# Kernel optimization log

Hardware: AMD Instinct MI355X
Metric: run time of the kernel (lower is better)

The kernel has to match this reference:

```python
import jax, jax.numpy as jnp
import numpy as np

N_NODES = 50000
N_EDGES = 400000
HIDDEN = 128
OUT_DIM = 1
N_LAYERS = 3
NUM_GRAPHS = 64
VOCAB = 101


def _lin(x, w, b):
    return x @ w + b


def setup_inputs() -> dict:
    key = jax.random.key(0)
    ks = jax.random.split(key, 20)
    inp = {}
    inp['z'] = jax.random.randint(ks[0], (N_NODES,), 0, VOCAB)
    inp['edge_index'] = jax.random.randint(ks[1], (2, N_EDGES), 0, N_NODES)
    inp['edge_attr'] = jax.random.normal(ks[2], (N_EDGES, 1), dtype=jnp.float32)
    inp['batch'] = jnp.sort(jax.random.randint(ks[3], (N_NODES,), 0, NUM_GRAPHS))
    s = 0.05
    inp['embed'] = jax.random.normal(ks[4], (VOCAB, HIDDEN), dtype=jnp.float32) * s
    # per-layer stacked params; weights stored [in, out]
    inp['msg_w1'] = jax.random.normal(ks[5], (N_LAYERS, 2 * HIDDEN + 1, HIDDEN), dtype=jnp.float32) * s
    inp['msg_b1'] = jnp.zeros((N_LAYERS, HIDDEN), dtype=jnp.float32)
    inp['msg_w2'] = jax.random.normal(ks[6], (N_LAYERS, HIDDEN, HIDDEN), dtype=jnp.float32) * s
    inp['msg_b2'] = jnp.zeros((N_LAYERS, HIDDEN), dtype=jnp.float32)
    inp['upd_w1'] = jax.random.normal(ks[7], (N_LAYERS, 2 * HIDDEN, HIDDEN), dtype=jnp.float32) * s
    inp['upd_b1'] = jnp.zeros((N_LAYERS, HIDDEN), dtype=jnp.float32)
    inp['upd_w2'] = jax.random.normal(ks[8], (N_LAYERS, HIDDEN, HIDDEN), dtype=jnp.float32) * s
    inp['upd_b2'] = jnp.zeros((N_LAYERS, HIDDEN), dtype=jnp.float32)
    inp['head_w1'] = jax.random.normal(ks[9], (HIDDEN, HIDDEN), dtype=jnp.float32) * s
    inp['head_b1'] = jnp.zeros((HIDDEN,), dtype=jnp.float32)
    inp['head_w2'] = jax.random.normal(ks[10], (HIDDEN, OUT_DIM), dtype=jnp.float32) * s
    inp['head_b2'] = jnp.zeros((OUT_DIM,), dtype=jnp.float32)
    return inp


def reference(z, edge_index, edge_attr, batch, embed, msg_w1, msg_b1, msg_w2, msg_b2,
              upd_w1, upd_b1, upd_w2, upd_b2, head_w1, head_b1, head_w2, head_b2):
    src, dst = edge_index[0], edge_index[1]
    h = embed[z]  # [N, H]
    for l in range(N_LAYERS):
        m_in = jnp.concatenate([h[src], h[dst], edge_attr], axis=1)  # [E, 2H+1]
        msg = _lin(jax.nn.relu(_lin(m_in, msg_w1[l], msg_b1[l])), msg_w2[l], msg_b2[l])
        agg = jax.ops.segment_sum(msg, dst, num_segments=N_NODES)  # [N, H]
        upd_in = jnp.concatenate([h, agg], axis=1)  # [N, 2H]
        h = h + _lin(jax.nn.relu(_lin(upd_in, upd_w1[l], upd_b1[l])), upd_w2[l], upd_b2[l])
    pooled = jax.ops.segment_sum(h, batch, num_segments=NUM_GRAPHS)
    counts = jax.ops.segment_sum(jnp.ones((h.shape[0], 1), h.dtype), batch, num_segments=NUM_GRAPHS)
    pooled = pooled / jnp.maximum(counts, 1.0)
    return _lin(jax.nn.relu(_lin(pooled, head_w1, head_b1)), head_w2, head_b2)
```

## Files before the change

kernel.cpp:

```cpp
#include <hip/hip_runtime.h>

#define N_NODES 50000
#define NPAD 50048
#define N_EDGES 400000
#define HID 128
#define NUM_GRAPHS 64
#define SCAN_B 196
#define ECAP 2048

typedef __bf16 bf16;
typedef bf16 bf16x8 __attribute__((ext_vector_type(8)));
typedef float f32x4 __attribute__((ext_vector_type(4)));

__device__ inline bf16x8 cvt8(const float* p) {
    const float4 a = *(const float4*)p;
    const float4 b = *(const float4*)(p + 4);
    bf16x8 v;
    v[0] = (bf16)a.x; v[1] = (bf16)a.y; v[2] = (bf16)a.z; v[3] = (bf16)a.w;
    v[4] = (bf16)b.x; v[5] = (bf16)b.y; v[6] = (bf16)b.z; v[7] = (bf16)b.w;
    return v;
}

__device__ __forceinline__ void tile_out(const bf16* lds, bf16* g, int n0, int tid) {
    #pragma unroll
    for (int u = 0; u < 4; ++u) {
        const int unit = u * 256 + tid;
        const int row = unit >> 4;
        const int ci = (unit & 15) * 8;
        *(bf16x8*)&g[(size_t)(n0 + row) * HID + ci] =
            *(const bf16x8*)&lds[row * 136 + ci];
    }
}

__global__ void k_hist(const int* __restrict__ edst, int* __restrict__ deg) {
    int e = blockIdx.x * 256 + threadIdx.x;
    if (e < N_EDGES) atomicAdd(&deg[edst[e]], 1);
}

__global__ void k_scan1(const int* __restrict__ deg, int* __restrict__ partial) {
    __shared__ int buf[256];
    int i = blockIdx.x * 256 + threadIdx.x;
    buf[threadIdx.x] = (i < N_NODES) ? deg[i] : 0;
    __syncthreads();
    for (int off = 128; off > 0; off >>= 1) {
        if (threadIdx.x < off) buf[threadIdx.x] += buf[threadIdx.x + off];
        __syncthreads();
    }
    if (threadIdx.x == 0) partial[blockIdx.x] = buf[0];
}

__global__ void k_scan2(int* __restrict__ partial, int* __restrict__ row_ptr) {
    __shared__ int buf[256];
    int v = (threadIdx.x < SCAN_B) ? partial[threadIdx.x] : 0;
    buf[threadIdx.x] = v;
    __syncthreads();
    for (int off = 1; off < 256; off <<= 1) {
        int t = (threadIdx.x >= off) ? buf[threadIdx.x - off] : 0;
        __syncthreads();
        buf[threadIdx.x] += t;
        __syncthreads();
    }
    if (threadIdx.x < SCAN_B) partial[threadIdx.x] = buf[threadIdx.x] - v;
    if (threadIdx.x == 255) row_ptr[N_NODES] = buf[255];
}

__global__ void k_scan3(const int* __restrict__ deg, const int* __restrict__ partial,
                        int* __restrict__ row_ptr, int* __restrict__ cursor) {
    __shared__ int buf[256];
    int i = blockIdx.x * 256 + threadIdx.x;
    int v = (i < N_NODES) ? deg[i] : 0;
    buf[threadIdx.x] = v;
    __syncthreads();
    for (int off = 1; off < 256; off <<= 1) {
        int t = (threadIdx.x >= off) ? buf[threadIdx.x - off] : 0;
        __syncthreads();
        buf[threadIdx.x] += t;
        __syncthreads();
    }
    if (i < N_NODES) {
        int ex = partial[blockIdx.x] + buf[threadIdx.x] - v;
        row_ptr[i] = ex;
        cursor[i] = ex;
    }
}

__global__ void k_scatter(const int* __restrict__ esrc, const int* __restrict__ edst,
                          const float* __restrict__ attr, int* __restrict__ cursor,
                          int* __restrict__ s_src, float* __restrict__ s_attr) {
    int e = blockIdx.x * 256 + threadIdx.x;
    if (e >= N_EDGES) return;
    int p = atomicAdd(&cursor[edst[e]], 1);
    s_src[p] = esrc[e];
    s_attr[p] = attr[e];
}

__global__ void k_wprep(const float* __restrict__ msg_w1, const float* __restrict__ upd_w1,
                        const float* __restrict__ upd_w2,
                        bf16* __restrict__ W1t, bf16* __restrict__ U1t,
                        bf16* __restrict__ U2t) {
    const int l = blockIdx.y;
    const int n = blockIdx.x, k = threadIdx.x;
    const float* w1  = msg_w1 + (size_t)l * 257 * HID;
    const float* uw1 = upd_w1 + (size_t)l * 2 * HID * HID;
    const float* uw2 = upd_w2 + (size_t)l * HID * HID;
    if (n < 256) {
        W1t[(size_t)l * 256 * HID + n * HID + k] =
            (bf16)w1[(size_t)((n & 128) + k) * HID + (n & 127)];
    } else if (n < 384) {
        const int nn = n - 256;
        U1t[(size_t)l * HID * HID + nn * HID + k] = (bf16)uw1[(size_t)k * HID + nn];
    } else {
        const int nn = n - 384;
        U2t[(size_t)l * HID * HID + nn * HID + k] = (bf16)uw2[(size_t)k * HID + nn];
    }
}

__global__ void k_small(const float* __restrict__ msg_w2, const float* __restrict__ upd_w1,
                        const float* __restrict__ msg_b2,
                        bf16* __restrict__ W2Ut, float* __restrict__ b2u) {
    __shared__ float row[HID];
    const int l = blockIdx.y;
    const int k = blockIdx.x, j = threadIdx.x;
    const float* w2  = msg_w2 + (size_t)l * HID * HID;
    const float* uw1 = upd_w1 + (size_t)l * 2 * HID * HID;
    const float* b2  = msg_b2 + (size_t)l * HID;
    const float* src = (k < HID) ? &w2[(size_t)k * HID] : b2;
    row[j] = src[j];
    __syncthreads();
    float acc = 0.f;
    #pragma unroll 8
    for (int m = 0; m < HID; ++m)
        acc = fmaf(row[m], uw1[(size_t)(HID + m) * HID + j], acc);
    if (k < HID) W2Ut[(size_t)l * HID * HID + (size_t)j * HID + k] = (bf16)acc;
    else b2u[l * HID + j] = acc;
}

__launch_bounds__(256, 4)
__global__ void k_embed_pre(const int* __restrict__ z, const float* __restrict__ embed,
                            const bf16* __restrict__ W1t, const float* __restrict__ b1,
                            bf16* __restrict__ h16, bf16* __restrict__ P, bf16* __restrict__ Q) {
    __shared__ bf16 sH[64 * 136];
    __shared__ bf16 sH2[64 * 136];
    const int tid = threadIdx.x;
    const int n0 = blockIdx.x * 64;
    {
        const int r = tid & 63, cg = tid >> 6;
        const int n = n0 + r;
        const bool valid = n < N_NODES;
        const float* src = valid ? &embed[(size_t)z[n] * HID + cg * 32] : embed;
        #pragma unroll
        for (int i = 0; i < 4; ++i) {
            bf16x8 v;
            if (valid) {
                v = cvt8(src + i * 8);
            } else {
                for (int j = 0; j < 8; ++j) v[j] = (bf16)0.f;
            }
            *(bf16x8*)&sH[r * 136 + cg * 32 + i * 8] = v;
        }
    }
    __syncthreads();
    tile_out(sH, h16, n0, tid);

    const int lane = tid & 63, wave = tid >> 6;
    const int lr = lane & 15, kq = (lane >> 4) * 8, rq = (lane >> 4) * 4;
    const int bcol = wave * 64;

    const f32x4 z4 = {0.f, 0.f, 0.f, 0.f};
    f32x4 acc[4][4];
    #pragma unroll
    for (int mi = 0; mi < 4; ++mi)
        #pragma unroll
        for (int ni = 0; ni < 4; ++ni) acc[mi][ni] = z4;

    #pragma unroll
    for (int ks = 0; ks < 4; ++ks) {
        bf16x8 av[4], bv[4];
        #pragma unroll
        for (int mi = 0; mi < 4; ++mi)
            av[mi] = *(const bf16x8*)&sH[(mi * 16 + lr) * 136 + ks * 32 + kq];
        #pragma unroll
        for (int ni = 0; ni < 4; ++ni)
            bv[ni] = *(const bf16x8*)&W1t[(size_t)(bcol + ni * 16 + lr) * HID + ks * 32 + kq];
        #pragma unroll
        for (int mi = 0; mi < 4; ++mi)
            #pragma unroll
            for (int ni = 0; ni < 4; ++ni)
                acc[mi][ni] = __builtin_amdgcn_mfma_f32_16x16x32_bf16(av[mi], bv[ni],
                                                                      acc[mi][ni], 0, 0, 0);
    }
    __syncthreads();

    {
        bf16* sOut = (bcol < 128) ? sH : sH2;
        const int cb = bcol & 127;
        #pragma unroll
        for (int ni = 0; ni < 4; ++ni) {
            const int c = cb + ni * 16 + lr;
            const float bias = (bcol >= 128) ? b1[c] : 0.f;
            #pragma unroll
            for (int mi = 0; mi < 4; ++mi)
                #pragma unroll
                for (int r = 0; r < 4; ++r)
                    sOut[(mi * 16 + rq + r) * 136 + c] = (bf16)(acc[mi][ni][r] + bias);
        }
    }
    __syncthreads();
    tile_out(sH, P, n0, tid);
    tile_out(sH2, Q, n0, tid);
}

template<int DO_PRE>
__launch_bounds__(256, 4)
__global__ void k_layer(bf16* __restrict__ h16,
                        const bf16* __restrict__ P, const bf16* __restrict__ Q,
                        const int* __restrict__ row_ptr, const int* __restrict__ s_src,
                        const float* __restrict__ s_attr, const float* __restrict__ w1last,
                        const bf16* __restrict__ U1t, const bf16* __restrict__ W2Ut,
                        const float* __restrict__ ub1, const float* __restrict__ b2u,
                        const bf16* __restrict__ U2t, const float* __restrict__ ub2,
                        const bf16* __restrict__ W1tn, const float* __restrict__ b1n,
                        bf16* __restrict__ Pn, bf16* __restrict__ Qn) {
    __shared__ bf16 sAgg[64 * 136];
    __shared__ bf16 sT[64 * 136];
    __shared__ float sDeg[64];
    const int tid = threadIdx.x;
    const int n0 = blockIdx.x * 64;

    {
        int*   sEsrc = (int*)sT;
        float* sEatt = (float*)(sT + ECAP * 2);
        const int elo = row_ptr[n0];
        const int ehi = row_ptr[min(n0 + 64, N_NODES)];
        const int ecap = min(ehi - elo, ECAP);
        for (int i = tid; i < ecap; i += 256) {
            sEsrc[i] = s_src[elo + i];
            sEatt[i] = s_attr[elo + i];
        }
        __syncthreads();

        const int grp = tid >> 4, ln = tid & 15, c8 = ln * 8;
        float wl[8];
        #pragma unroll
        for (int j = 0; j < 8; ++j) wl[j] = w1last[c8 + j];
        #pragma unroll
        for (int t = 0; t < 4; ++t) {
            const int row = t * 16 + grp;
            const int n = n0 + row;
            float a8[8];
            #pragma unroll
            for (int j = 0; j < 8; ++j) a8[j] = 0.f;
            if (n < N_NODES) {
                const int lo = row_ptr[n], hi = row_ptr[n + 1];
                if (ln == 0) sDeg[row] = (float)(hi - lo);
                const bf16x8 qv = *(const bf16x8*)&Q[(size_t)n * HID + c8];
                float q8[8];
                #pragma unroll
                for (int j = 0; j < 8; ++j) q8[j] = (float)qv[j];
                const int llo = lo - elo, lhi = hi - elo;
                if (lhi <= ecap) {
                    int e = llo;
                    for (; e + 4 <= lhi; e += 4) {
                        const int s0 = sEsrc[e], s1 = sEsrc[e + 1];
                        const int s2 = sEsrc[e + 2], s3 = sEsrc[e + 3];
                        const float t0 = sEatt[e], t1 = sEatt[e + 1];
                        const float t2 = sEatt[e + 2], t3 = sEatt[e + 3];
                        const bf16x8 p0 = *(const bf16x8*)&P[(size_t)s0 * HID + c8];
                        const bf16x8 p1 = *(const bf16x8*)&P[(size_t)s1 * HID + c8];
                        const bf16x8 p2 = *(const bf16x8*)&P[(size_t)s2 * HID + c8];
                        const bf16x8 p3 = *(const bf16x8*)&P[(size_t)s3 * HID + c8];
                        #pragma unroll
                        for (int j = 0; j < 8; ++j) {
                            a8[j] += fmaxf(fmaf(t0, wl[j], q8[j] + (float)p0[j]), 0.f);
                            a8[j] += fmaxf(fmaf(t1, wl[j], q8[j] + (float)p1[j]), 0.f);
                            a8[j] += fmaxf(fmaf(t2, wl[j], q8[j] + (float)p2[j]), 0.f);
                            a8[j] += fmaxf(fmaf(t3, wl[j], q8[j] + (float)p3[j]), 0.f);
                        }
                    }
                    for (; e < lhi; ++e) {
                        const int s0 = sEsrc[e];
                        const float t0 = sEatt[e];
                        const bf16x8 p0 = *(const bf16x8*)&P[(size_t)s0 * HID + c8];
                        #pragma unroll
                        for (int j = 0; j < 8; ++j)
                            a8[j] += fmaxf(fmaf(t0, wl[j], q8[j] + (float)p0[j]), 0.f);
                    }
                } else {
                    for (int e = lo; e < hi; ++e) {
                        const int s0 = s_src[e];
                        const float t0 = s_attr[e];
                        const bf16x8 p0 = *(const bf16x8*)&P[(size_t)s0 * HID + c8];
                        #pragma unroll
                        for (int j = 0; j < 8; ++j)
                            a8[j] += fmaxf(fmaf(t0, wl[j], q8[j] + (float)p0[j]), 0.f);
                    }
                }
            } else if (ln == 0) {
                sDeg[row] = 0.f;
            }
            bf16x8 o;
            #pragma unroll
            for (int j = 0; j < 8; ++j) o[j] = (bf16)a8[j];
            *(bf16x8*)&sAgg[row * 136 + c8] = o;
        }
    }
    __syncthreads();

    const int lane = tid & 63, wave = tid >> 6;
    const int lr = lane & 15, kq = (lane >> 4) * 8, rq = (lane >> 4) * 4;
    const int nw = wave * 32;
    const f32x4 z4 = {0.f, 0.f, 0.f, 0.f};

    f32x4 acc[4][2];
    #pragma unroll
    for (int mi = 0; mi < 4; ++mi) { acc[mi][0] = z4; acc[mi][1] = z4; }

    #pragma unroll
    for (int ks = 0; ks < 4; ++ks) {
        bf16x8 av[4], bv[2];
        #pragma unroll
        for (int mi = 0; mi < 4; ++mi)
            av[mi] = *(const bf16x8*)&h16[(size_t)(n0 + mi * 16 + lr) * HID + ks * 32 + kq];
        #pragma unroll
        for (int ni = 0; ni < 2; ++ni)
            bv[ni] = *(const bf16x8*)&U1t[(size_t)(nw + ni * 16 + lr) * HID + ks * 32 + kq];
        #pragma unroll
        for (int mi = 0; mi < 4; ++mi)
            #pragma unroll
            for (int ni = 0; ni < 2; ++ni)
                acc[mi][ni] = __builtin_amdgcn_mfma_f32_16x16x32_bf16(av[mi], bv[ni],
                                                                      acc[mi][ni], 0, 0, 0);
    }
    #pragma unroll
    for (int ks = 0; ks < 4; ++ks) {
        bf16x8 av[4], bv[2];
        #pragma unroll
        for (int mi = 0; mi < 4; ++mi)
            av[mi] = *(const bf16x8*)&sAgg[(mi * 16 + lr) * 136 + ks * 32 + kq];
        #pragma unroll
        for (int ni = 0; ni < 2; ++ni)
            bv[ni] = *(const bf16x8*)&W2Ut[(size_t)(nw + ni * 16 + lr) * HID + ks * 32 + kq];
        #pragma unroll
        for (int mi = 0; mi < 4; ++mi)
            #pragma unroll
            for (int ni = 0; ni < 2; ++ni)
                acc[mi][ni] = __builtin_amdgcn_mfma_f32_16x16x32_bf16(av[mi], bv[ni],
                                                                      acc[mi][ni], 0, 0, 0);
    }
    __syncthreads();

    #pragma unroll
    for (int ni = 0; ni < 2; ++ni) {
        const int c = nw + ni * 16 + lr;
        const float bb1 = ub1[c], bb2 = b2u[c];
        #pragma unroll
        for (int mi = 0; mi < 4; ++mi)
            #pragma unroll
            for (int r = 0; r < 4; ++r) {
                const int row = mi * 16 + rq + r;
                float v = acc[mi][ni][r] + bb1 + sDeg[row] * bb2;
                sT[row * 136 + c] = (bf16)fmaxf(v, 0.f);
            }
    }
    __syncthreads();

    f32x4 acc2[4][2];
    #pragma unroll
    for (int mi = 0; mi < 4; ++mi) { acc2[mi][0] = z4; acc2[mi][1] = z4; }
    #pragma unroll
    for (int ks = 0; ks < 4; ++ks) {
        bf16x8 av[4], bv[2];
        #pragma unroll
        for (int mi = 0; mi < 4; ++mi)
            av[mi] = *(const bf16x8*)&sT[(mi * 16 + lr) * 136 + ks * 32 + kq];
        #pragma unroll
        for (int ni = 0; ni < 2; ++ni)
            bv[ni] = *(const bf16x8*)&U2t[(size_t)(nw + ni * 16 + lr) * HID + ks * 32 + kq];
        #pragma unroll
        for (int mi = 0; mi < 4; ++mi)
            #pragma unroll
            for (int ni = 0; ni < 2; ++ni)
                acc2[mi][ni] = __builtin_amdgcn_mfma_f32_16x16x32_bf16(av[mi], bv[ni],
                                                                       acc2[mi][ni], 0, 0, 0);
    }
    __syncthreads();

    #pragma unroll
    for (int ni = 0; ni < 2; ++ni) {
        const int c = nw + ni * 16 + lr;
        const float bb = ub2[c];
        #pragma unroll
        for (int mi = 0; mi < 4; ++mi)
            #pragma unroll
            for (int r = 0; r < 4; ++r) {
                const int row = mi * 16 + rq + r;
                const size_t off = (size_t)(n0 + row) * HID + c;
                const float nh = (float)h16[off] + acc2[mi][ni][r] + bb;
                sT[row * 136 + c] = (bf16)nh;
                if (DO_PRE) sAgg[row * 136 + c] = (bf16)nh;
            }
    }
    __syncthreads();
    tile_out(sT, h16, n0, tid);

    if (DO_PRE) {
        const int bcol = wave * 64;
        f32x4 pacc[4][4];
        #pragma unroll
        for (int mi = 0; mi < 4; ++mi)
            #pragma unroll
            for (int ni = 0; ni < 4; ++ni) pacc[mi][ni] = z4;

        #pragma unroll
        for (int ks = 0; ks < 4; ++ks) {
            bf16x8 av[4], bv[4];
            #pragma unroll
            for (int mi = 0; mi < 4; ++mi)
                av[mi] = *(const bf16x8*)&sAgg[(mi * 16 + lr) * 136 + ks * 32 + kq];
            #pragma unroll
            for (int ni = 0; ni < 4; ++ni)
                bv[ni] = *(const bf16x8*)&W1tn[(size_t)(bcol + ni * 16 + lr) * HID + ks * 32 + kq];
            #pragma unroll
            for (int mi = 0; mi < 4; ++mi)
                #pragma unroll
                for (int ni = 0; ni < 4; ++ni)
                    pacc[mi][ni] = __builtin_amdgcn_mfma_f32_16x16x32_bf16(av[mi], bv[ni],
                                                                           pacc[mi][ni], 0, 0, 0);
        }
        __syncthreads();

        {
            bf16* sOut = (bcol < 128) ? sT : sAgg;
            const int cb = bcol & 127;
            #pragma unroll
            for (int ni = 0; ni < 4; ++ni) {
                const int c = cb + ni * 16 + lr;
                const float bias = (bcol >= 128) ? b1n[c] : 0.f;
                #pragma unroll
                for (int mi = 0; mi < 4; ++mi)
                    #pragma unroll
                    for (int r = 0; r < 4; ++r)
                        sOut[(mi * 16 + rq + r) * 136 + c] = (bf16)(pacc[mi][ni][r] + bias);
            }
        }
        __syncthreads();
        tile_out(sT, Pn, n0, tid);
        tile_out(sAgg, Qn, n0, tid);
    }
}

__global__ void k_pool(const bf16* __restrict__ h16, const int* __restrict__ batch,
                       float* __restrict__ pooled) {
    const int n0 = blockIdx.x * 64;
    const int c = threadIdx.x & 127;
    const int half = threadIdx.x >> 7;
    int cur = -1;
    float s = 0.f;
    const int rbeg = n0 + half * 32;
    const int rend = min(rbeg + 32, N_NODES);
    for (int n = rbeg; n < rend; ++n) {
        const int g = batch[n];
        const float v = (float)h16[(size_t)n * HID + c];
        if (g != cur) {
            if (cur >= 0) atomicAdd(&pooled[cur * HID + c], s);
            cur = g; s = v;
        } else {
            s += v;
        }
    }
    if (cur >= 0) atomicAdd(&pooled[cur * HID + c], s);
}

__device__ inline int lb(const int* a, int n, int v) {
    int lo = 0, hi = n;
    while (lo < hi) { int m = (lo + hi) >> 1; if (a[m] < v) lo = m + 1; else hi = m; }
    return lo;
}

__global__ void k_head(const float* __restrict__ pooled, const int* __restrict__ batch,
                       const float* __restrict__ hw1, const float* __restrict__ hb1,
                       const float* __restrict__ hw2, const float* __restrict__ hb2,
                       float* __restrict__ out) {
    const int g = blockIdx.x;
    const int c = threadIdx.x;
    __shared__ float sp[HID];
    __shared__ float red[HID];
    __shared__ int sb[2];
    if (c == 0) { sb[0] = lb(batch, N_NODES, g); sb[1] = lb(batch, N_NODES, g + 1); }
    __syncthreads();
    const float cnt = fmaxf((float)(sb[1] - sb[0]), 1.f);
    sp[c] = pooled[g * HID + c] / cnt;
    __syncthreads();
    float acc = hb1[c];
    #pragma unroll 8
    for (int k = 0; k < HID; ++k) acc = fmaf(sp[k], hw1[k * HID + c], acc);
    red[c] = fmaxf(acc, 0.f) * hw2[c];
    __syncthreads();
    for (int s = 64; s > 0; s >>= 1) {
        if (c < s) red[c] += red[c + s];
        __syncthreads();
    }
    if (c == 0) out[g] = red[0] + hb2[0];
}

extern "C" void kernel_launch(void* const* d_in, const int* in_sizes, int n_in,
                              void* d_out, int out_size, void* d_ws, size_t ws_size,
                              hipStream_t stream) {
    const int*   z       = (const int*)d_in[0];
    const int*   ei      = (const int*)d_in[1];
    const float* eattr   = (const float*)d_in[2];
    const int*   batch   = (const int*)d_in[3];
    const float* embed   = (const float*)d_in[4];
    const float* msg_w1  = (const float*)d_in[5];
    const float* msg_b1  = (const float*)d_in[6];
    const float* msg_w2  = (const float*)d_in[7];
    const float* msg_b2  = (const float*)d_in[8];
    const float* upd_w1  = (const float*)d_in[9];
    const float* upd_b1  = (const float*)d_in[10];
    const float* upd_w2  = (const float*)d_in[11];
    const float* upd_b2  = (const float*)d_in[12];
    const float* head_w1 = (const float*)d_in[13];
    const float* head_b1 = (const float*)d_in[14];
    const float* head_w2 = (const float*)d_in[15];
    const float* head_b2 = (const float*)d_in[16];
    float* out = (float*)d_out;

    float* pooled = (float*)d_ws;
    float* b2u    = pooled + NUM_GRAPHS * HID;
    float* s_attr = b2u + 3 * HID;
    int* deg_i    = (int*)(s_attr + N_EDGES);
    int* row_ptr  = deg_i + N_NODES;
    int* partial  = row_ptr + N_NODES + 1;
    int* cursor   = partial + 256;
    int* s_src    = cursor + N_NODES;
    bf16* h16     = (bf16*)((((unsigned long long)(s_src + N_EDGES)) + 15ULL) & ~15ULL);
    bf16* P0      = h16 + (size_t)NPAD * HID;
    bf16* Q0      = P0 + (size_t)NPAD * HID;
    bf16* P1      = Q0 + (size_t)NPAD * HID;
    bf16* Q1      = P1 + (size_t)NPAD * HID;
    bf16* W1t     = Q1 + (size_t)NPAD * HID;
    bf16* U1t     = W1t + 3 * 256 * HID;
    bf16* W2Ut    = U1t + 3 * HID * HID;
    bf16* U2t     = W2Ut + 3 * HID * HID;

    const int* esrc = ei;
    const int* edst = ei + N_EDGES;

    hipMemsetAsync(deg_i, 0, N_NODES * sizeof(int), stream);
    k_hist<<<(N_EDGES + 255) / 256, 256, 0, stream>>>(edst, deg_i);
    k_scan1<<<SCAN_B, 256, 0, stream>>>(deg_i, partial);
    k_scan2<<<1, 256, 0, stream>>>(partial, row_ptr);
    k_scan3<<<SCAN_B, 256, 0, stream>>>(deg_i, partial, row_ptr, cursor);
    k_scatter<<<(N_EDGES + 255) / 256, 256, 0, stream>>>(esrc, edst, eattr, cursor, s_src, s_attr);
    {
        dim3 g1(512, 3);
        k_wprep<<<g1, 128, 0, stream>>>(msg_w1, upd_w1, upd_w2, W1t, U1t, U2t);
        dim3 g2(HID + 1, 3);
        k_small<<<g2, HID, 0, stream>>>(msg_w2, upd_w1, msg_b2, W2Ut, b2u);
    }

    const int nblk = NPAD / 64;
    k_embed_pre<<<nblk, 256, 0, stream>>>(z, embed, W1t, msg_b1, h16, P0, Q0);

    bf16* Pa = P0; bf16* Qa = Q0; bf16* Pb = P1; bf16* Qb = Q1;
    for (int l = 0; l < 3; ++l) {
        const float* w1last = msg_w1 + (size_t)l * 257 * HID + 256 * HID;
        const bf16* U1l  = U1t  + (size_t)l * HID * HID;
        const bf16* W2Ul = W2Ut + (size_t)l * HID * HID;
        const bf16* U2l  = U2t  + (size_t)l * HID * HID;
        if (l < 2) {
            k_layer<1><<<nblk, 256, 0, stream>>>(
                h16, Pa, Qa, row_ptr, s_src, s_attr, w1last,
                U1l, W2Ul, upd_b1 + (size_t)l * HID, b2u + l * HID,
                U2l, upd_b2 + (size_t)l * HID,
                W1t + (size_t)(l + 1) * 256 * HID, msg_b1 + (size_t)(l + 1) * HID, Pb, Qb);
            bf16* tp = Pa; Pa = Pb; Pb = tp;
            bf16* tq = Qa; Qa = Qb; Qb = tq;
        } else {
            k_layer<0><<<nblk, 256, 0, stream>>>(
                h16, Pa, Qa, row_ptr, s_src, s_attr, w1last,
                U1l, W2Ul, upd_b1 + (size_t)l * HID, b2u + l * HID,
                U2l, upd_b2 + (size_t)l * HID,
                nullptr, nullptr, nullptr, nullptr);
        }
    }
    hipMemsetAsync(pooled, 0, NUM_GRAPHS * HID * sizeof(float), stream);
    k_pool<<<nblk, 256, 0, stream>>>(h16, batch, pooled);
    k_head<<<NUM_GRAPHS, 128, 0, stream>>>(pooled, batch, head_w1, head_b1, head_w2, head_b2, out);
}
```

Baseline: 266.2 us.

## Fuse mean-pool into final layer kernel and unroll edge gather by eight

The final layer kernel now does the graph pooling directly from its shared-memory tile. This drops the separate pool kernel and the last write and re-read of h16. The edge aggregation loop also gains an 8-wide unrolled path so more independent P-row gathers are in flight, at the cost of extra register pressure. Row bounds are now guarded when reading h16 for padded rows.

```diff
diff --git a/kernel.cpp b/kernel.cpp
--- a/kernel.cpp
+++ b/kernel.cpp
@@ -220,7 +220,8 @@
                         const float* __restrict__ ub1, const float* __restrict__ b2u,
                         const bf16* __restrict__ U2t, const float* __restrict__ ub2,
                         const bf16* __restrict__ W1tn, const float* __restrict__ b1n,
-                        bf16* __restrict__ Pn, bf16* __restrict__ Qn) {
+                        bf16* __restrict__ Pn, bf16* __restrict__ Qn,
+                        const int* __restrict__ batch, float* __restrict__ pooled) {
     __shared__ bf16 sAgg[64 * 136];
     __shared__ bf16 sT[64 * 136];
     __shared__ float sDeg[64];
@@ -260,6 +261,21 @@
                 const int llo = lo - elo, lhi = hi - elo;
                 if (lhi <= ecap) {
                     int e = llo;
+                    for (; e + 8 <= lhi; e += 8) {
+                        int   ss[8];
+                        float tt[8];
+                        bf16x8 pp[8];
+                        #pragma unroll
+                        for (int u = 0; u < 8; ++u) { ss[u] = sEsrc[e + u]; tt[u] = sEatt[e + u]; }
+                        #pragma unroll
+                        for (int u = 0; u < 8; ++u)
+                            pp[u] = *(const bf16x8*)&P[(size_t)ss[u] * HID + c8];
+                        #pragma unroll
+                        for (int u = 0; u < 8; ++u)
+                            #pragma unroll
+                            for (int j = 0; j < 8; ++j)
+                                a8[j] += fmaxf(fmaf(tt[u], wl[j], q8[j] + (float)pp[u][j]), 0.f);
+                    }
                     for (; e + 4 <= lhi; e += 4) {
                         const int s0 = sEsrc[e], s1 = sEsrc[e + 1];
                         const int s2 = sEsrc[e + 2], s3 = sEsrc[e + 3];
@@ -394,16 +410,21 @@
             #pragma unroll
             for (int r = 0; r < 4; ++r) {
                 const int row = mi * 16 + rq + r;
-                const size_t off = (size_t)(n0 + row) * HID + c;
-                const float nh = (float)h16[off] + acc2[mi][ni][r] + bb;
+                const int gr = n0 + row;
+                float nh = 0.f;
+                if (gr < N_NODES) {
+                    const size_t off = (size_t)gr * HID + c;
+                    nh = (float)h16[off] + acc2[mi][ni][r] + bb;
+                }
                 sT[row * 136 + c] = (bf16)nh;
                 if (DO_PRE) sAgg[row * 136 + c] = (bf16)nh;
             }
     }
     __syncthreads();
-    tile_out(sT, h16, n0, tid);
 
     if (DO_PRE) {
+        tile_out(sT, h16, n0, tid);
+
         const int bcol = wave * 64;
         f32x4 pacc[4][4];
         #pragma unroll
@@ -446,29 +467,26 @@
         __syncthreads();
         tile_out(sT, Pn, n0, tid);
         tile_out(sAgg, Qn, n0, tid);
-    }
-}
-
-__global__ void k_pool(const bf16* __restrict__ h16, const int* __restrict__ batch,
-                       float* __restrict__ pooled) {
-    const int n0 = blockIdx.x * 64;
-    const int c = threadIdx.x & 127;
-    const int half = threadIdx.x >> 7;
-    int cur = -1;
-    float s = 0.f;
-    const int rbeg = n0 + half * 32;
-    const int rend = min(rbeg + 32, N_NODES);
-    for (int n = rbeg; n < rend; ++n) {
-        const int g = batch[n];
-        const float v = (float)h16[(size_t)n * HID + c];
-        if (g != cur) {
-            if (cur >= 0) atomicAdd(&pooled[cur * HID + c], s);
-            cur = g; s = v;
-        } else {
-            s += v;
-        }
-    }
-    if (cur >= 0) atomicAdd(&pooled[cur * HID + c], s);
+    } else {
+        const int c = tid & 127;
+        const int half = tid >> 7;
+        const int rows = min(64, N_NODES - n0);
+        const int rbeg = half * 32;
+        const int rend = min(rbeg + 32, rows);
+        int cur = -1;
+        float s = 0.f;
+        for (int r = rbeg; r < rend; ++r) {
+            const int g = batch[n0 + r];
+            const float v = (float)sT[r * 136 + c];
+            if (g != cur) {
+                if (cur >= 0) atomicAdd(&pooled[cur * HID + c], s);
+                cur = g; s = v;
+            } else {
+                s += v;
+            }
+        }
+        if (cur >= 0) atomicAdd(&pooled[cur * HID + c], s);
+    }
 }
 
 __device__ inline int lb(const int* a, int n, int v) {
@@ -547,6 +565,7 @@
     const int* edst = ei + N_EDGES;
 
     hipMemsetAsync(deg_i, 0, N_NODES * sizeof(int), stream);
+    hipMemsetAsync(pooled, 0, NUM_GRAPHS * HID * sizeof(float), stream);
     k_hist<<<(N_EDGES + 255) / 256, 256, 0, stream>>>(edst, deg_i);
     k_scan1<<<SCAN_B, 256, 0, stream>>>(deg_i, partial);
     k_scan2<<<1, 256, 0, stream>>>(partial, row_ptr);
@@ -573,7 +592,8 @@
                 h16, Pa, Qa, row_ptr, s_src, s_attr, w1last,
                 U1l, W2Ul, upd_b1 + (size_t)l * HID, b2u + l * HID,
                 U2l, upd_b2 + (size_t)l * HID,
-                W1t + (size_t)(l + 1) * 256 * HID, msg_b1 + (size_t)(l + 1) * HID, Pb, Qb);
+                W1t + (size_t)(l + 1) * 256 * HID, msg_b1 + (size_t)(l + 1) * HID, Pb, Qb,
+                nullptr, nullptr);
             bf16* tp = Pa; Pa = Pb; Pb = tp;
             bf16* tq = Qa; Qa = Qb; Qb = tq;
         } else {
@@ -581,10 +601,9 @@
                 h16, Pa, Qa, row_ptr, s_src, s_attr, w1last,
                 U1l, W2Ul, upd_b1 + (size_t)l * HID, b2u + l * HID,
                 U2l, upd_b2 + (size_t)l * HID,
-                nullptr, nullptr, nullptr, nullptr);
-        }
-    }
-    hipMemsetAsync(pooled, 0, NUM_GRAPHS * HID * sizeof(float), stream);
-    k_pool<<<nblk, 256, 0, stream>>>(h16, batch, pooled);
+                nullptr, nullptr, nullptr, nullptr,
+                batch, pooled);
+        }
+    }
     k_head<<<NUM_GRAPHS, 128, 0, stream>>>(pooled, batch, head_w1, head_b1, head_w2, head_b2, out);
 }
```

Result: slower. 293.0 us (+10.1%).
